# Performance work log

Measured on AMD Instinct MI355X. Metric: run time of the kernel, lower is better.

The kernel has to match this reference:

```python
import jax, jax.numpy as jnp
import numpy as np

B, N, K = 4, 4096, 10   # batch, num points, ED_nsample
SA, ED = 128, 4          # SA_conv_out, ED_conv_out


def _bn_pack(key, C):
    # rows: gamma, beta, running_mean, running_var (eval-mode BatchNorm1d)
    kg, kb, km, kv = jax.random.split(key, 4)
    g = 1.0 + 0.1 * jax.random.normal(kg, (C,))
    b = 0.1 * jax.random.normal(kb, (C,))
    m = 0.1 * jax.random.normal(km, (C,))
    v = jax.random.uniform(kv, (C,), minval=0.5, maxval=1.5)
    return jnp.stack([g, b, m, v])


def _conv_params(key, o, c):
    kw, kb = jax.random.split(key)
    return (jax.random.normal(kw, (o, c)) * (1.0 / np.sqrt(c)),
            0.01 * jax.random.normal(kb, (o,)))


def setup_inputs() -> dict:
    key = jax.random.key(0)
    ks = iter(jax.random.split(key, 32))
    inp = {}
    inp['pointcloud'] = jax.random.normal(next(ks), (B, N, 3), dtype=jnp.float32)
    inp['h1'] = jax.random.normal(next(ks), (B, SA, N), dtype=jnp.float32)      # Pointnet_Backbone output
    inp['h2'] = jax.random.normal(next(ks), (B, 1024, N), dtype=jnp.float32)    # DGCNN output
    shapes = {'dg1': (256, 1024), 'dg2': (64, 256), 'dg3': (32, 64),
              'c1': (512, 160), 'c2': (256, 512), 'c3': (128, 256), 'f': (128, 132)}
    for name, (o, c) in shapes.items():
        W, b = _conv_params(next(ks), o, c)
        inp['W_' + name], inp['b_' + name] = W, b
        inp['bn_' + name] = _bn_pack(next(ks), o)
    inp['W_ed1'] = jax.random.normal(next(ks), (ED, 3)) * 0.5
    inp['b_ed1'] = 0.01 * jax.random.normal(next(ks), (ED,))
    inp['W_ed2'] = jax.random.normal(next(ks), (ED, ED)) * 0.5
    inp['b_ed2'] = 0.01 * jax.random.normal(next(ks), (ED,))
    inp['numpoints'] = N
    return inp


def _bn1d(x, p, eps=1e-5):
    # x: [B, C, N]; p rows: gamma, beta, mean, var
    g, b, m, v = p
    inv = g * jax.lax.rsqrt(v + eps)
    return x * inv[:, None] + (b - m * inv)[:, None]


def _conv1(x, W, b):
    # 1x1 Conv1d == channel matmul. x: [B,C,N], W: [O,C]
    return jnp.einsum('oc,bcn->bon', W, x) + b[:, None]


def reference(pointcloud, h1, h2,
              W_dg1, b_dg1, bn_dg1, W_dg2, b_dg2, bn_dg2, W_dg3, b_dg3, bn_dg3,
              W_c1, b_c1, bn_c1, W_c2, b_c2, bn_c2, W_c3, b_c3, bn_c3,
              W_f, b_f, bn_f, W_ed1, b_ed1, W_ed2, b_ed2, numpoints):
    relu = jax.nn.relu
    xyz = pointcloud[..., :3]  # [B,N,3]

    # DGCNN feature reduction: 1024 -> 256 -> 64 -> 32
    h2_ = relu(_bn1d(_conv1(h2, W_dg1, b_dg1), bn_dg1))
    h2_ = relu(_bn1d(_conv1(h2_, W_dg2, b_dg2), bn_dg2))
    h2_ = relu(_bn1d(_conv1(h2_, W_dg3, b_dg3), bn_dg3))

    # fused feature: 160 -> 512 -> 256 -> 128
    f = jnp.concatenate([h1, h2_], axis=1)
    f_ = relu(_bn1d(_conv1(f, W_c1, b_c1), bn_c1))
    f_ = relu(_bn1d(_conv1(f_, W_c2, b_c2), bn_c2))
    f_ = relu(_bn1d(_conv1(f_, W_c3, b_c3), bn_c3))

    # knn_point: K nearest neighbors of each point within its cloud
    sq = jnp.sum(xyz * xyz, axis=-1)  # [B,N]
    d = sq[:, :, None] + sq[:, None, :] - 2.0 * jnp.einsum('bnd,bmd->bnm', xyz, xyz)
    _, idx = jax.lax.top_k(-d, K)  # [B,N,K]
    nbr = jax.vmap(lambda p, i: p[i])(xyz, idx)  # [B,N,K,3]

    # per-point 3x3 covariance + eigenvalues
    c = nbr - jnp.mean(nbr, axis=2, keepdims=True)
    cov = jnp.einsum('bnki,bnkj->bnij', c, c) / K  # [B,N,3,3]
    ev = jnp.linalg.eigvalsh(cov)  # [B,N,3] ascending

    # sub3_ED: Linear(3,4) -> ReLU -> Linear(4,4)
    ef = relu(ev @ W_ed1.T + b_ed1) @ W_ed2.T + b_ed2  # [B,N,4]
    ef_t = ef.transpose(0, 2, 1)  # [B,4,N]

    z = jnp.concatenate([f_, ef_t], axis=1)  # [B,132,N]
    z_ = relu(_bn1d(_conv1(z, W_f, b_f), bn_f))  # [B,128,N]
    return (xyz, z_, h1, h2_, ef_t)
```

## Files before the change

kernel.cpp:

```cpp
#include <hip/hip_runtime.h>
#include <hip/hip_bf16.h>
#include <math.h>

typedef __hip_bfloat16 bf16;

#define BB 4
#define NN 4096
#define KNB 10
#define KQ 16
#define KCAP 64

typedef __bf16 bfv8 __attribute__((ext_vector_type(8)));
typedef float  f32x4 __attribute__((ext_vector_type(4)));

__device__ __forceinline__ float ldT(const float* p) { return *p; }
__device__ __forceinline__ float ldT(const bf16* p)  { return __bfloat162float(*p); }
__device__ __forceinline__ void  stT(float* p, float v) { *p = v; }
__device__ __forceinline__ void  stT(bf16* p,  float v) { *p = __float2bfloat16(v); }

__device__ __forceinline__ unsigned short f2us(float x) {
  union { bf16 h; unsigned short u; } cv;
  cv.h = __float2bfloat16(x);
  return cv.u;
}

__device__ __forceinline__ void ld8bits(const float* p, unsigned short* s) {
  const float4 a = *(const float4*)p;
  const float4 b = *(const float4*)(p + 4);
  s[0] = f2us(a.x); s[1] = f2us(a.y); s[2] = f2us(a.z); s[3] = f2us(a.w);
  s[4] = f2us(b.x); s[5] = f2us(b.y); s[6] = f2us(b.z); s[7] = f2us(b.w);
}
__device__ __forceinline__ void ld8bits(const bf16* p, unsigned short* s) {
  const uint2 a = *(const uint2*)p;
  const uint2 b = *(const uint2*)(p + 4);
  s[0] = a.x & 0xffff; s[1] = a.x >> 16; s[2] = a.y & 0xffff; s[3] = a.y >> 16;
  s[4] = b.x & 0xffff; s[5] = b.x >> 16; s[6] = b.y & 0xffff; s[7] = b.y >> 16;
}

__device__ __forceinline__ bfv8 ldfrag(const unsigned short* p) {
  union { uint4 u; bfv8 v; } t;
  t.u = *(const uint4*)p;
  return t.v;
}

__global__ void k_sniff(const unsigned int* __restrict__ pcw, int* __restrict__ flag) {
  if (blockIdx.x == 0 && threadIdx.x == 0) {
    int hits = 0;
    for (int i = 0; i < 64; ++i) {
      unsigned int e = (pcw[i] >> 7) & 0xFF;
      if (e >= 100 && e <= 140) ++hits;
    }
    *flag = (hits >= 40) ? 1 : 0;
  }
}

template <class TI, class TO>
__global__ void k_prep(const int* __restrict__ flag, int want,
                       const TI* __restrict__ pc, float* __restrict__ xyz,
                       float4* __restrict__ pts4, TO* __restrict__ out0) {
  if (flag && *flag != want) return;
  int i = blockIdx.x * blockDim.x + threadIdx.x;
  if (i >= BB * NN) return;
  float x = ldT(pc + i * 3 + 0), y = ldT(pc + i * 3 + 1), z = ldT(pc + i * 3 + 2);
  xyz[i * 3 + 0] = x; xyz[i * 3 + 1] = y; xyz[i * 3 + 2] = z;
  const float nrm = fmaf(x, x, fmaf(y, y, z * z));
  pts4[i] = make_float4(x, y, z, nrm);
  stT(out0 + i * 3 + 0, x); stT(out0 + i * 3 + 1, y); stT(out0 + i * 3 + 2, z);
}

template <class TI, class TO>
__global__ void k_h1(const int* __restrict__ flag, int want,
                     const TI* __restrict__ h1, TO* __restrict__ out2,
                     bf16* __restrict__ fbuf) {
  if (flag && *flag != want) return;
  const int per8 = 128 * NN / 8;
  int g = blockIdx.x * blockDim.x + threadIdx.x;
  if (g >= BB * per8) return;
  const int b = g / per8;
  const int e = (g - b * per8) * 8;
  const size_t src = (size_t)b * (128 * NN) + e;
  bf16* fb = fbuf + (size_t)b * 160 * NN + e;
  if constexpr (sizeof(TI) == 2) {
    const uint4 u = *(const uint4*)(h1 + src);
    *(uint4*)(out2 + src) = u;
    *(uint4*)fb = u;
  } else {
    const float4 a = *(const float4*)(h1 + src);
    const float4 c = *(const float4*)(h1 + src + 4);
    *(float4*)(out2 + src) = a;
    *(float4*)(out2 + src + 4) = c;
    uint4 u;
    u.x = (unsigned)f2us(a.x) | ((unsigned)f2us(a.y) << 16);
    u.y = (unsigned)f2us(a.z) | ((unsigned)f2us(a.w) << 16);
    u.z = (unsigned)f2us(c.x) | ((unsigned)f2us(c.y) << 16);
    u.w = (unsigned)f2us(c.z) | ((unsigned)f2us(c.w) << 16);
    *(uint4*)fb = u;
  }
}

__global__ __launch_bounds__(256, 4) void k_knn(const float4* __restrict__ pts4,
                                                int* __restrict__ idxout) {
  __shared__ float smin[256][KQ + 1];
  __shared__ float stau[KQ];
  __shared__ float sd[KQ][KCAP];
  __shared__ int   si[KQ][KCAP];
  __shared__ unsigned int scnt[KQ];
  const int tid = threadIdx.x;
  const int b = blockIdx.y;
  const int nBase = blockIdx.x * KQ;
  const float4* pb = pts4 + (size_t)b * NN;
  if (tid < KQ) scnt[tid] = 0u;

  float qx[KQ], qy[KQ], qz[KQ], qn[KQ];
  #pragma unroll
  for (int q = 0; q < KQ; ++q) {
    const float4 p = pb[nBase + q];
    qx[q] = p.x; qy[q] = p.y; qz[q] = p.z; qn[q] = p.w;
  }
  #pragma unroll
  for (int q = 0; q < KQ; ++q)
    asm volatile("" : "+v"(qx[q]), "+v"(qy[q]), "+v"(qz[q]), "+v"(qn[q]));

  float mv[KQ];
  #pragma unroll
  for (int q = 0; q < KQ; ++q) mv[q] = 1e30f;
  {
    float4 cA = pb[tid];
    #pragma unroll
    for (int it = 0; it < 16; ++it) {
      const float4 cB = (it + 1 < 16) ? pb[(it + 1) * 256 + tid] : cA;
      #pragma unroll
      for (int q = 0; q < KQ; ++q) {
        const float dot = fmaf(qx[q], cA.x, fmaf(qy[q], cA.y, qz[q] * cA.z));
        const float d = (qn[q] + cA.w) - 2.0f * dot;
        mv[q] = fminf(mv[q], d);
      }
      cA = cB;
    }
  }
  #pragma unroll
  for (int q = 0; q < KQ; ++q) smin[tid][q] = mv[q];
  __syncthreads();

  if (tid < KQ) {
    float arr[KNB];
    #pragma unroll
    for (int t = 0; t < KNB; ++t) arr[t] = 1e30f;
    for (int t = 0; t < 256; ++t) {
      const float v = smin[t][tid];
      if (v < arr[KNB - 1]) {
        arr[KNB - 1] = v;
        #pragma unroll
        for (int u = KNB - 1; u > 0; --u)
          if (arr[u] < arr[u - 1]) { const float tm = arr[u]; arr[u] = arr[u - 1]; arr[u - 1] = tm; }
      }
    }
    stau[tid] = arr[KNB - 1];
  }
  __syncthreads();
  float tq[KQ];
  #pragma unroll
  for (int q = 0; q < KQ; ++q) tq[q] = stau[q];

  {
    float4 cA = pb[tid];
    #pragma unroll
    for (int it = 0; it < 16; ++it) {
      const float4 cB = (it + 1 < 16) ? pb[(it + 1) * 256 + tid] : cA;
      const int j = it * 256 + tid;
      #pragma unroll
      for (int q = 0; q < KQ; ++q) {
        const float dot = fmaf(qx[q], cA.x, fmaf(qy[q], cA.y, qz[q] * cA.z));
        const float d = (qn[q] + cA.w) - 2.0f * dot;
        if (d <= tq[q]) {
          const unsigned int pos = atomicAdd(&scnt[q], 1u);
          if (pos < KCAP) { sd[q][pos] = d; si[q][pos] = j; }
        }
      }
      cA = cB;
    }
  }
  __syncthreads();

  if (tid < KQ) {
    const int qq = tid;
    const int nq = nBase + qq;
    int* op = idxout + ((size_t)b * NN + nq) * KNB;
    const unsigned int m = scnt[qq];
    float dk[KNB]; int ik[KNB];
    #pragma unroll
    for (int t = 0; t < KNB; ++t) { dk[t] = 1e30f; ik[t] = NN; }
    if (m <= KCAP) {
      for (unsigned int e = 0; e < m; ++e) {
        const float d = sd[qq][e];
        const int j = si[qq][e];
        if (d < dk[KNB - 1] || (d == dk[KNB - 1] && j < ik[KNB - 1])) {
          dk[KNB - 1] = d; ik[KNB - 1] = j;
          #pragma unroll
          for (int t = KNB - 1; t > 0; --t) {
            if (dk[t] < dk[t - 1] || (dk[t] == dk[t - 1] && ik[t] < ik[t - 1])) {
              const float td = dk[t]; dk[t] = dk[t - 1]; dk[t - 1] = td;
              const int ti = ik[t]; ik[t] = ik[t - 1]; ik[t - 1] = ti;
            }
          }
        }
      }
    } else {
      const float4 pQ = pb[nq];
      for (int j = 0; j < NN; ++j) {
        const float4 c = pb[j];
        const float dot = fmaf(pQ.x, c.x, fmaf(pQ.y, c.y, pQ.z * c.z));
        const float d = (pQ.w + c.w) - 2.0f * dot;
        if (d < dk[KNB - 1] || (d == dk[KNB - 1] && j < ik[KNB - 1])) {
          dk[KNB - 1] = d; ik[KNB - 1] = j;
          #pragma unroll
          for (int t = KNB - 1; t > 0; --t) {
            if (dk[t] < dk[t - 1] || (dk[t] == dk[t - 1] && ik[t] < ik[t - 1])) {
              const float td = dk[t]; dk[t] = dk[t - 1]; dk[t - 1] = td;
              const int ti = ik[t]; ik[t] = ik[t - 1]; ik[t - 1] = ti;
            }
          }
        }
      }
    }
    #pragma unroll
    for (int t = 0; t < KNB; ++t) op[t] = ik[t];
  }
}

template <class TP, class TO>
__global__ void k_ef(const int* __restrict__ flag, int want,
                     const float* __restrict__ xyz, const int* __restrict__ idxin,
                     const TP* __restrict__ W1, const TP* __restrict__ b1,
                     const TP* __restrict__ W2, const TP* __restrict__ b2,
                     TO* __restrict__ out4, bf16* __restrict__ zbuf) {
  if (flag && *flag != want) return;
  int i = blockIdx.x * blockDim.x + threadIdx.x;
  if (i >= BB * NN) return;
  int b = i / NN, n = i - b * NN;
  const float* xb = xyz + (size_t)b * NN * 3;
  const int* id = idxin + (size_t)i * KNB;
  double px[KNB], py[KNB], pz[KNB];
  double mx = 0, my = 0, mz = 0;
  #pragma unroll
  for (int k = 0; k < KNB; ++k) {
    int j = id[k];
    px[k] = (double)xb[j * 3 + 0];
    py[k] = (double)xb[j * 3 + 1];
    pz[k] = (double)xb[j * 3 + 2];
    mx += px[k]; my += py[k]; mz += pz[k];
  }
  mx /= KNB; my /= KNB; mz /= KNB;
  double c00 = 0, c01 = 0, c02 = 0, c11 = 0, c12 = 0, c22 = 0;
  #pragma unroll
  for (int k = 0; k < KNB; ++k) {
    double dx = px[k] - mx, dy = py[k] - my, dz = pz[k] - mz;
    c00 += dx * dx; c01 += dx * dy; c02 += dx * dz;
    c11 += dy * dy; c12 += dy * dz; c22 += dz * dz;
  }
  c00 /= KNB; c01 /= KNB; c02 /= KNB; c11 /= KNB; c12 /= KNB; c22 /= KNB;
  double e0, e1, e2;
  {
    double p1 = c01 * c01 + c02 * c02 + c12 * c12;
    double q = (c00 + c11 + c22) / 3.0;
    double d0 = c00 - q, d1 = c11 - q, d2 = c22 - q;
    double p2 = d0 * d0 + d1 * d1 + d2 * d2 + 2.0 * p1;
    if (p2 <= 0.0) {
      e0 = e1 = e2 = q;
    } else {
      double p = sqrt(p2 / 6.0);
      double ip = 1.0 / p;
      double b00 = d0 * ip, b11 = d1 * ip, b22 = d2 * ip;
      double b01 = c01 * ip, b02 = c02 * ip, b12 = c12 * ip;
      double det = b00 * (b11 * b22 - b12 * b12)
                 - b01 * (b01 * b22 - b12 * b02)
                 + b02 * (b01 * b12 - b11 * b02);
      double r = 0.5 * det;
      r = fmin(1.0, fmax(-1.0, r));
      double phi = acos(r) / 3.0;
      double lmax = q + 2.0 * p * cos(phi);
      double lmin = q + 2.0 * p * cos(phi + 2.0943951023931953);
      e0 = lmin; e2 = lmax; e1 = 3.0 * q - lmax - lmin;
    }
  }
  float ev0 = (float)e0, ev1 = (float)e1, ev2 = (float)e2;
  float h[4];
  #pragma unroll
  for (int o = 0; o < 4; ++o) {
    float t = ev0 * ldT(W1 + o * 3 + 0) + ev1 * ldT(W1 + o * 3 + 1)
            + ev2 * ldT(W1 + o * 3 + 2) + ldT(b1 + o);
    h[o] = fmaxf(t, 0.f);
  }
  #pragma unroll
  for (int j = 0; j < 4; ++j) {
    float t = h[0] * ldT(W2 + j * 4 + 0) + h[1] * ldT(W2 + j * 4 + 1)
            + h[2] * ldT(W2 + j * 4 + 2) + h[3] * ldT(W2 + j * 4 + 3)
            + ldT(b2 + j);
    stT(out4 + ((size_t)b * 4 + j) * NN + n, t);
    zbuf[((size_t)b * 132 + 128 + j) * NN + n] = __float2bfloat16(t);
  }
}

template <class TX, class TP, class TO>
__global__ __launch_bounds__(256) void k_gemm(
    const int* __restrict__ flag, int want,
    const TX* __restrict__ X, int C,
    const TP* __restrict__ W, const TP* __restrict__ bias,
    const TP* __restrict__ bn, int O,
    TO* __restrict__ Yout, int YRo, int yoffo,
    bf16* __restrict__ Ybuf, int YRb, int yoffb) {
  if (flag && *flag != want) return;
  __shared__ __align__(16) unsigned short Ws[64][72];
  __shared__ __align__(16) unsigned short Xs[64][72];
  const int tid  = threadIdx.x;
  const int lane = tid & 63;
  const int wv   = tid >> 6;
  const int wr = wv >> 1, wc = wv & 1;
  const int l15 = lane & 15, lg = lane >> 4;
  const int nBase = blockIdx.x * 64;
  const int oBase = blockIdx.y * 64;
  const int b = blockIdx.z;
  const TX* Xb = X + (size_t)b * C * NN;

  f32x4 acc[2][2];
  #pragma unroll
  for (int m = 0; m < 2; ++m)
    #pragma unroll
    for (int n = 0; n < 2; ++n) acc[m][n] = (f32x4){0.f, 0.f, 0.f, 0.f};

  const int wo  = tid >> 3;
  const int wc0 = (tid & 7) << 3;
  const int xc  = tid >> 3;
  const int xn0 = (tid & 7) << 3;

  for (int cb = 0; cb < C; cb += 64) {
    #pragma unroll
    for (int h = 0; h < 2; ++h) {
      const int o  = wo + h * 32;
      const int go = oBase + o, gc = cb + wc0;
      const int crem = C - gc;
      unsigned short s[8];
      if (go < O && crem >= 8) {
        ld8bits(W + (size_t)go * C + gc, s);
      } else {
        #pragma unroll
        for (int j = 0; j < 8; ++j)
          s[j] = (go < O && j < crem) ? f2us(ldT(W + (size_t)go * C + gc + j))
                                      : (unsigned short)0;
      }
      uint4 u;
      u.x = (unsigned)s[0] | ((unsigned)s[1] << 16);
      u.y = (unsigned)s[2] | ((unsigned)s[3] << 16);
      u.z = (unsigned)s[4] | ((unsigned)s[5] << 16);
      u.w = (unsigned)s[6] | ((unsigned)s[7] << 16);
      *(uint4*)&Ws[o][wc0] = u;
    }
    #pragma unroll
    for (int h = 0; h < 2; ++h) {
      const int c  = xc + h * 32;
      const int gc = cb + c;
      unsigned short s[8];
      if (gc < C) {
        ld8bits(Xb + (size_t)gc * NN + nBase + xn0, s);
      } else {
        #pragma unroll
        for (int j = 0; j < 8; ++j) s[j] = 0;
      }
      const int xcol = c ^ xn0;
      #pragma unroll
      for (int j = 0; j < 8; ++j) Xs[xn0 + j][xcol] = s[j];
    }
    __syncthreads();
    #pragma unroll
    for (int kk = 0; kk < 2; ++kk) {
      bfv8 af[2], xf[2];
      #pragma unroll
      for (int m = 0; m < 2; ++m)
        af[m] = ldfrag(&Ws[wr * 32 + m * 16 + l15][kk * 32 + lg * 8]);
      #pragma unroll
      for (int n = 0; n < 2; ++n) {
        const int nl  = wc * 32 + n * 16 + l15;
        const int col = (kk * 32 + lg * 8) ^ (((nl >> 3) & 7) << 3);
        xf[n] = ldfrag(&Xs[nl][col]);
      }
      #pragma unroll
      for (int m = 0; m < 2; ++m)
        #pragma unroll
        for (int n = 0; n < 2; ++n)
          acc[m][n] = __builtin_amdgcn_mfma_f32_16x16x32_bf16(af[m], xf[n], acc[m][n], 0, 0, 0);
    }
    __syncthreads();
  }

  #pragma unroll
  for (int m = 0; m < 2; ++m) {
    const int ob = oBase + wr * 32 + m * 16 + lg * 4;
    #pragma unroll
    for (int r = 0; r < 4; ++r) {
      const int oo = ob + r;
      if (oo >= O) continue;
      const float bc  = ldT(bias + oo);
      const float g   = ldT(bn + oo);
      const float bbv = ldT(bn + O + oo);
      const float mm  = ldT(bn + 2 * O + oo);
      const float vv  = ldT(bn + 3 * O + oo);
      const float inv = g / sqrtf(vv + 1e-5f);
      const float sh  = bbv - mm * inv;
      #pragma unroll
      for (int n = 0; n < 2; ++n) {
        const int nn2 = nBase + wc * 32 + n * 16 + l15;
        const float rv = fmaxf((acc[m][n][r] + bc) * inv + sh, 0.f);
        if (Yout) stT(Yout + ((size_t)b * YRo + yoffo + oo) * NN + nn2, rv);
        if (Ybuf) Ybuf[((size_t)b * YRb + yoffb + oo) * NN + nn2] = __float2bfloat16(rv);
      }
    }
  }
}

template <class TI>
static void launch_prep(int want, const int* flag, void* const* d_in, void* d_out,
                        hipStream_t stream, float* xyz, float4* pts4) {
  typedef TI TO;
  const TI* pc = (const TI*)d_in[0];
  TO* out0 = (TO*)d_out;
  k_prep<TI, TO><<<dim3((BB * NN + 255) / 256), 256, 0, stream>>>(flag, want, pc, xyz, pts4, out0);
}

template <class TI>
static void launch_rest(int want, const int* flag,
                        void* const* d_in, void* d_out, hipStream_t stream,
                        float* xyz, int* idx,
                        bf16* t512, bf16* t256, bf16* t64, bf16* fbuf, bf16* zbuf) {
  typedef TI TO;
  const TI* h1    = (const TI*)d_in[1];
  const TI* h2    = (const TI*)d_in[2];
  const TI* W_dg1 = (const TI*)d_in[3];  const TI* b_dg1 = (const TI*)d_in[4];  const TI* bn_dg1 = (const TI*)d_in[5];
  const TI* W_dg2 = (const TI*)d_in[6];  const TI* b_dg2 = (const TI*)d_in[7];  const TI* bn_dg2 = (const TI*)d_in[8];
  const TI* W_dg3 = (const TI*)d_in[9];  const TI* b_dg3 = (const TI*)d_in[10]; const TI* bn_dg3 = (const TI*)d_in[11];
  const TI* W_c1  = (const TI*)d_in[12]; const TI* b_c1  = (const TI*)d_in[13]; const TI* bn_c1  = (const TI*)d_in[14];
  const TI* W_c2  = (const TI*)d_in[15]; const TI* b_c2  = (const TI*)d_in[16]; const TI* bn_c2  = (const TI*)d_in[17];
  const TI* W_c3  = (const TI*)d_in[18]; const TI* b_c3  = (const TI*)d_in[19]; const TI* bn_c3  = (const TI*)d_in[20];
  const TI* W_f   = (const TI*)d_in[21]; const TI* b_f   = (const TI*)d_in[22]; const TI* bn_f   = (const TI*)d_in[23];
  const TI* W_ed1 = (const TI*)d_in[24]; const TI* b_ed1 = (const TI*)d_in[25];
  const TI* W_ed2 = (const TI*)d_in[26]; const TI* b_ed2 = (const TI*)d_in[27];

  TO* out  = (TO*)d_out;
  TO* out1 = out + 49152;
  TO* out2 = out1 + 2097152;
  TO* out3 = out2 + 2097152;
  TO* out4 = out3 + 524288;

  dim3 blk(256);
  k_h1<TI, TO><<<dim3((BB * 128 * NN / 8 + 255) / 256), 256, 0, stream>>>(flag, want, h1, out2, fbuf);
  k_gemm<TI, TI, TO><<<dim3(64, 4, BB), blk, 0, stream>>>(flag, want, h2, 1024, W_dg1, b_dg1, bn_dg1, 256,
                                                          (TO*)nullptr, 0, 0, t256, 256, 0);
  k_gemm<bf16, TI, TO><<<dim3(64, 1, BB), blk, 0, stream>>>(flag, want, t256, 256, W_dg2, b_dg2, bn_dg2, 64,
                                                            (TO*)nullptr, 0, 0, t64, 64, 0);
  k_gemm<bf16, TI, TO><<<dim3(64, 1, BB), blk, 0, stream>>>(flag, want, t64, 64, W_dg3, b_dg3, bn_dg3, 32,
                                                            out3, 32, 0, fbuf, 160, 128);
  k_gemm<bf16, TI, TO><<<dim3(64, 8, BB), blk, 0, stream>>>(flag, want, fbuf, 160, W_c1, b_c1, bn_c1, 512,
                                                            (TO*)nullptr, 0, 0, t512, 512, 0);
  k_ef<TI, TO><<<dim3((BB * NN + 255) / 256), 256, 0, stream>>>(flag, want, xyz, idx, W_ed1, b_ed1, W_ed2, b_ed2, out4, zbuf);
  k_gemm<bf16, TI, TO><<<dim3(64, 4, BB), blk, 0, stream>>>(flag, want, t512, 512, W_c2, b_c2, bn_c2, 256,
                                                            (TO*)nullptr, 0, 0, t256, 256, 0);
  k_gemm<bf16, TI, TO><<<dim3(64, 2, BB), blk, 0, stream>>>(flag, want, t256, 256, W_c3, b_c3, bn_c3, 128,
                                                            (TO*)nullptr, 0, 0, zbuf, 132, 0);
  k_gemm<bf16, TI, TO><<<dim3(64, 2, BB), blk, 0, stream>>>(flag, want, zbuf, 132, W_f, b_f, bn_f, 128,
                                                            out1, 128, 0, (bf16*)nullptr, 0, 0);
}

extern "C" void kernel_launch(void* const* d_in, const int* in_sizes, int n_in,
                              void* d_out, int out_size, void* d_ws, size_t ws_size,
                              hipStream_t stream) {
  char* ws = (char*)d_ws;
  int*    flag = (int*)(ws + 0);
  float*  xyz  = (float*)(ws + 1024);
  int*    idx  = (int*)(ws + 328704);
  bf16*   t512 = (bf16*)(ws + 1048576);
  bf16*   t256 = (bf16*)(ws + 17825792);
  bf16*   t64  = (bf16*)(ws + 26214400);
  bf16*   fbuf = (bf16*)(ws + 28311552);
  bf16*   zbuf = (bf16*)(ws + 33554432);
  float4* pts4 = (float4*)(ws + 1048576);

  int mode = -1;
  if (in_sizes) {
    if (in_sizes[0] == (int)(BB * NN * 3 * sizeof(float))) mode = 0;
    else if (in_sizes[0] == (int)(BB * NN * 3 * sizeof(bf16))) mode = 1;
  }

  if (mode < 0) {
    k_sniff<<<1, 64, 0, stream>>>((const unsigned int*)d_in[0], flag);
    launch_prep<float>(0, flag, d_in, d_out, stream, xyz, pts4);
    launch_prep<bf16>(1, flag, d_in, d_out, stream, xyz, pts4);
  } else if (mode == 0) {
    launch_prep<float>(0, nullptr, d_in, d_out, stream, xyz, pts4);
  } else {
    launch_prep<bf16>(1, nullptr, d_in, d_out, stream, xyz, pts4);
  }

  k_knn<<<dim3(NN / KQ, BB), 256, 0, stream>>>(pts4, idx);

  if (mode != 1) launch_rest<float>(0, mode < 0 ? flag : nullptr, d_in, d_out, stream,
                                    xyz, idx, t512, t256, t64, fbuf, zbuf);
  if (mode != 0) launch_rest<bf16>(1, mode < 0 ? flag : nullptr, d_in, d_out, stream,
                                   xyz, idx, t512, t256, t64, fbuf, zbuf);
}
```

Baseline: 386.8 us.

## Horizontally fuse independent kernels into combined launches by block-index dispatch

Turns the KNN, h1-copy, dg1 GEMM, edge-feature and c2 GEMM kernels into device-function bodies that take explicit block coordinates and a shared-memory pointer. Two new kernels dispatch on block index: one runs KNN, the first DGCNN GEMM and the h1 copy together, the other runs the eigenvalue feature pass alongside the c2 GEMM. The aim is to let independent work share the GPU at the same time and to cut launch count and tail idle time. In exchange, all fused blocks reserve the largest shared-memory footprint and use the stricter launch bounds, which may limit occupancy for the GEMM blocks.

After: 848.3 us. 2.19x slower.

```diff
diff --git a/kernel.cpp b/kernel.cpp
--- a/kernel.cpp
+++ b/kernel.cpp
@@ -69,12 +69,10 @@
 }
 
 template <class TI, class TO>
-__global__ void k_h1(const int* __restrict__ flag, int want,
-                     const TI* __restrict__ h1, TO* __restrict__ out2,
-                     bf16* __restrict__ fbuf) {
-  if (flag && *flag != want) return;
+__device__ __forceinline__ void h1_body(int blk, const TI* __restrict__ h1,
+                                        TO* __restrict__ out2, bf16* __restrict__ fbuf) {
   const int per8 = 128 * NN / 8;
-  int g = blockIdx.x * blockDim.x + threadIdx.x;
+  int g = blk * 256 + threadIdx.x;
   if (g >= BB * per8) return;
   const int b = g / per8;
   const int e = (g - b * per8) * 8;
@@ -98,16 +96,17 @@
   }
 }
 
-__global__ __launch_bounds__(256, 4) void k_knn(const float4* __restrict__ pts4,
-                                                int* __restrict__ idxout) {
-  __shared__ float smin[256][KQ + 1];
-  __shared__ float stau[KQ];
-  __shared__ float sd[KQ][KCAP];
-  __shared__ int   si[KQ][KCAP];
-  __shared__ unsigned int scnt[KQ];
+__device__ __forceinline__ void knn_body(char* smem, int bx, int by,
+                                         const float4* __restrict__ pts4,
+                                         int* __restrict__ idxout) {
+  float (*smin)[KQ + 1] = (float (*)[KQ + 1])smem;
+  float* stau = (float*)(smem + 17408);
+  float (*sd)[KCAP] = (float (*)[KCAP])(smem + 17472);
+  int   (*si)[KCAP] = (int (*)[KCAP])(smem + 21568);
+  unsigned int* scnt = (unsigned int*)(smem + 25664);
   const int tid = threadIdx.x;
-  const int b = blockIdx.y;
-  const int nBase = blockIdx.x * KQ;
+  const int b = by;
+  const int nBase = bx * KQ;
   const float4* pb = pts4 + (size_t)b * NN;
   if (tid < KQ) scnt[tid] = 0u;
 
@@ -229,13 +228,12 @@
 }
 
 template <class TP, class TO>
-__global__ void k_ef(const int* __restrict__ flag, int want,
-                     const float* __restrict__ xyz, const int* __restrict__ idxin,
-                     const TP* __restrict__ W1, const TP* __restrict__ b1,
-                     const TP* __restrict__ W2, const TP* __restrict__ b2,
-                     TO* __restrict__ out4, bf16* __restrict__ zbuf) {
-  if (flag && *flag != want) return;
-  int i = blockIdx.x * blockDim.x + threadIdx.x;
+__device__ __forceinline__ void ef_body(int blk,
+                                        const float* __restrict__ xyz, const int* __restrict__ idxin,
+                                        const TP* __restrict__ W1, const TP* __restrict__ b1,
+                                        const TP* __restrict__ W2, const TP* __restrict__ b2,
+                                        TO* __restrict__ out4, bf16* __restrict__ zbuf) {
+  int i = blk * 256 + threadIdx.x;
   if (i >= BB * NN) return;
   int b = i / NN, n = i - b * NN;
   const float* xb = xyz + (size_t)b * NN * 3;
@@ -302,24 +300,23 @@
 }
 
 template <class TX, class TP, class TO>
-__global__ __launch_bounds__(256) void k_gemm(
-    const int* __restrict__ flag, int want,
+__device__ __forceinline__ void gemm_body(
+    char* smem, int bx, int by, int bz,
     const TX* __restrict__ X, int C,
     const TP* __restrict__ W, const TP* __restrict__ bias,
     const TP* __restrict__ bn, int O,
     TO* __restrict__ Yout, int YRo, int yoffo,
     bf16* __restrict__ Ybuf, int YRb, int yoffb) {
-  if (flag && *flag != want) return;
-  __shared__ __align__(16) unsigned short Ws[64][72];
-  __shared__ __align__(16) unsigned short Xs[64][72];
+  unsigned short (*Ws)[72] = (unsigned short (*)[72])smem;
+  unsigned short (*Xs)[72] = (unsigned short (*)[72])(smem + 9216);
   const int tid  = threadIdx.x;
   const int lane = tid & 63;
   const int wv   = tid >> 6;
   const int wr = wv >> 1, wc = wv & 1;
   const int l15 = lane & 15, lg = lane >> 4;
-  const int nBase = blockIdx.x * 64;
-  const int oBase = blockIdx.y * 64;
-  const int b = blockIdx.z;
+  const int nBase = bx * 64;
+  const int oBase = by * 64;
+  const int b = bz;
   const TX* Xb = X + (size_t)b * C * NN;
 
   f32x4 acc[2][2];
@@ -417,6 +414,66 @@
   }
 }
 
+template <class TX, class TP, class TO>
+__global__ __launch_bounds__(256) void k_gemm(
+    const int* __restrict__ flag, int want,
+    const TX* __restrict__ X, int C,
+    const TP* __restrict__ W, const TP* __restrict__ bias,
+    const TP* __restrict__ bn, int O,
+    TO* __restrict__ Yout, int YRo, int yoffo,
+    bf16* __restrict__ Ybuf, int YRb, int yoffb) {
+  if (flag && *flag != want) return;
+  __shared__ __align__(16) char smem[18432];
+  gemm_body<TX, TP, TO>(smem, blockIdx.x, blockIdx.y, blockIdx.z,
+                        X, C, W, bias, bn, O, Yout, YRo, yoffo, Ybuf, YRb, yoffb);
+}
+
+template <class TI, class TO>
+__global__ __launch_bounds__(256, 4) void k_fat1(
+    const int* __restrict__ flag, int want,
+    const float4* __restrict__ pts4, int* __restrict__ idxout,
+    const TI* __restrict__ h1, TO* __restrict__ out2, bf16* __restrict__ fbuf,
+    const TI* __restrict__ h2, const TI* __restrict__ W1, const TI* __restrict__ b1,
+    const TI* __restrict__ bn1, bf16* __restrict__ t256) {
+  __shared__ __align__(16) char smem[25728];
+  const int bid = blockIdx.x;
+  if (bid < 1024) {
+    knn_body(smem, bid & 255, bid >> 8, pts4, idxout);
+  } else if (bid < 2048) {
+    if (flag && *flag != want) return;
+    const int r = bid - 1024;
+    gemm_body<TI, TI, TO>(smem, r & 63, (r >> 6) & 3, r >> 8,
+                          h2, 1024, W1, b1, bn1, 256,
+                          (TO*)nullptr, 0, 0, t256, 256, 0);
+  } else {
+    if (flag && *flag != want) return;
+    h1_body<TI, TO>(bid - 2048, h1, out2, fbuf);
+  }
+}
+
+template <class TI, class TO>
+__global__ __launch_bounds__(256, 4) void k_fat2(
+    const int* __restrict__ flag, int want,
+    const float* __restrict__ xyz, const int* __restrict__ idxin,
+    const TI* __restrict__ W_ed1, const TI* __restrict__ b_ed1,
+    const TI* __restrict__ W_ed2, const TI* __restrict__ b_ed2,
+    TO* __restrict__ out4, bf16* __restrict__ zbuf,
+    const bf16* __restrict__ t512, const TI* __restrict__ W_c2,
+    const TI* __restrict__ b_c2, const TI* __restrict__ bn_c2,
+    bf16* __restrict__ t256) {
+  __shared__ __align__(16) char smem[18432];
+  if (flag && *flag != want) return;
+  const int bid = blockIdx.x;
+  if (bid < 64) {
+    ef_body<TI, TO>(bid, xyz, idxin, W_ed1, b_ed1, W_ed2, b_ed2, out4, zbuf);
+  } else {
+    const int r = bid - 64;
+    gemm_body<bf16, TI, TO>(smem, r & 63, (r >> 6) & 3, r >> 8,
+                            t512, 512, W_c2, b_c2, bn_c2, 256,
+                            (TO*)nullptr, 0, 0, t256, 256, 0);
+  }
+}
+
 template <class TI>
 static void launch_prep(int want, const int* flag, void* const* d_in, void* d_out,
                         hipStream_t stream, float* xyz, float4* pts4) {
@@ -429,7 +486,7 @@
 template <class TI>
 static void launch_rest(int want, const int* flag,
                         void* const* d_in, void* d_out, hipStream_t stream,
-                        float* xyz, int* idx,
+                        float* xyz, float4* pts4, int* idx,
                         bf16* t512, bf16* t256, bf16* t64, bf16* fbuf, bf16* zbuf) {
   typedef TI TO;
   const TI* h1    = (const TI*)d_in[1];
@@ -451,18 +508,18 @@
   TO* out4 = out3 + 524288;
 
   dim3 blk(256);
-  k_h1<TI, TO><<<dim3((BB * 128 * NN / 8 + 255) / 256), 256, 0, stream>>>(flag, want, h1, out2, fbuf);
-  k_gemm<TI, TI, TO><<<dim3(64, 4, BB), blk, 0, stream>>>(flag, want, h2, 1024, W_dg1, b_dg1, bn_dg1, 256,
-                                                          (TO*)nullptr, 0, 0, t256, 256, 0);
+  k_fat1<TI, TO><<<dim3(3072), blk, 0, stream>>>(flag, want, pts4, idx,
+                                                 h1, out2, fbuf,
+                                                 h2, W_dg1, b_dg1, bn_dg1, t256);
   k_gemm<bf16, TI, TO><<<dim3(64, 1, BB), blk, 0, stream>>>(flag, want, t256, 256, W_dg2, b_dg2, bn_dg2, 64,
                                                             (TO*)nullptr, 0, 0, t64, 64, 0);
   k_gemm<bf16, TI, TO><<<dim3(64, 1, BB), blk, 0, stream>>>(flag, want, t64, 64, W_dg3, b_dg3, bn_dg3, 32,
                                                             out3, 32, 0, fbuf, 160, 128);
   k_gemm<bf16, TI, TO><<<dim3(64, 8, BB), blk, 0, stream>>>(flag, want, fbuf, 160, W_c1, b_c1, bn_c1, 512,
                                                             (TO*)nullptr, 0, 0, t512, 512, 0);
-  k_ef<TI, TO><<<dim3((BB * NN + 255) / 256), 256, 0, stream>>>(flag, want, xyz, idx, W_ed1, b_ed1, W_ed2, b_ed2, out4, zbuf);
-  k_gemm<bf16, TI, TO><<<dim3(64, 4, BB), blk, 0, stream>>>(flag, want, t512, 512, W_c2, b_c2, bn_c2, 256,
-                                                            (TO*)nullptr, 0, 0, t256, 256, 0);
+  k_fat2<TI, TO><<<dim3(1088), blk, 0, stream>>>(flag, want, xyz, idx,
+                                                 W_ed1, b_ed1, W_ed2, b_ed2, out4, zbuf,
+                                                 t512, W_c2, b_c2, bn_c2, t256);
   k_gemm<bf16, TI, TO><<<dim3(64, 2, BB), blk, 0, stream>>>(flag, want, t256, 256, W_c3, b_c3, bn_c3, 128,
                                                             (TO*)nullptr, 0, 0, zbuf, 132, 0);
   k_gemm<bf16, TI, TO><<<dim3(64, 2, BB), blk, 0, stream>>>(flag, want, zbuf, 132, W_f, b_f, bn_f, 128,
@@ -493,16 +550,13 @@
     k_sniff<<<1, 64, 0, stream>>>((const unsigned int*)d_in[0], flag);
     launch_prep<float>(0, flag, d_in, d_out, stream, xyz, pts4);
     launch_prep<bf16>(1, flag, d_in, d_out, stream, xyz, pts4);
+    launch_rest<float>(0, flag, d_in, d_out, stream, xyz, pts4, idx, t512, t256, t64, fbuf, zbuf);
+    launch_rest<bf16>(1, flag, d_in, d_out, stream, xyz, pts4, idx, t512, t256, t64, fbuf, zbuf);
   } else if (mode == 0) {
     launch_prep<float>(0, nullptr, d_in, d_out, stream, xyz, pts4);
+    launch_rest<float>(0, nullptr, d_in, d_out, stream, xyz, pts4, idx, t512, t256, t64, fbuf, zbuf);
   } else {
     launch_prep<bf16>(1, nullptr, d_in, d_out, stream, xyz, pts4);
-  }
-
-  k_knn<<<dim3(NN / KQ, BB), 256, 0, stream>>>(pts4, idx);
-
-  if (mode != 1) launch_rest<float>(0, mode < 0 ? flag : nullptr, d_in, d_out, stream,
-                                    xyz, idx, t512, t256, t64, fbuf, zbuf);
-  if (mode != 0) launch_rest<bf16>(1, mode < 0 ? flag : nullptr, d_in, d_out, stream,
-                                   xyz, idx, t512, t256, t64, fbuf, zbuf);
-}
+    launch_rest<bf16>(1, nullptr, d_in, d_out, stream, xyz, pts4, idx, t512, t256, t64, fbuf, zbuf);
+  }
+}
```
